# Optimization experiments

Hardware: AMD Instinct MI355X
Metric: run time of the kernel (lower is better)

## Reference

```python
import jax, jax.numpy as jnp
import numpy as np

N, D = 65536, 1024
EPS = 1e-12  # matches torch F.normalize default eps

def setup_inputs() -> dict:
    key = jax.random.key(0)
    k1, k2 = jax.random.split(key)
    premise = jax.random.normal(k1, (N, D), dtype=jnp.float32)
    hypothesis = jax.random.normal(k2, (N, D), dtype=jnp.float32)
    return {"premise": premise, "hypothesis": hypothesis}

def _l2_normalize(x):
    # torch.nn.functional.normalize(p=2, dim=-1): x / max(||x||, eps)
    norm = jnp.sqrt(jnp.sum(x * x, axis=-1, keepdims=True))
    return x / jnp.maximum(norm, EPS)

def reference(premise, hypothesis):
    # handle the [N,3,D] flattening branch of the original
    if premise.ndim == 3 and hypothesis.ndim == 3 and premise.shape[1] == 3 and hypothesis.shape[1] == 3:
        premise = premise.reshape(premise.shape[0], -1)
        hypothesis = hypothesis.reshape(hypothesis.shape[0], -1)
    p = _l2_normalize(premise)
    h = _l2_normalize(hypothesis)
    # diag(p @ h.T) == per-row dot product; avoid materializing NxN matrix
    return jnp.sum(p * h, axis=-1)
```

## Files before the change

### kernel.cpp

```cpp
#include <hip/hip_runtime.h>
#include <hip/hip_bf16.h>

#define D 1024
#define WAVES_PER_BLOCK 4

__global__ __launch_bounds__(256) void CosineSimilarity_76785425318088_kernel(
    const float* __restrict__ premise,
    const float* __restrict__ hypothesis,
    float* __restrict__ out,
    int n_rows) {
    const int wave = threadIdx.x >> 6;
    const int lane = threadIdx.x & 63;
    const int row = blockIdx.x * WAVES_PER_BLOCK + wave;
    if (row >= n_rows) return;

    const float4* __restrict__ prow = reinterpret_cast<const float4*>(premise    + (size_t)row * D);
    const float4* __restrict__ hrow = reinterpret_cast<const float4*>(hypothesis + (size_t)row * D);

    float dot = 0.f, pp = 0.f, hh = 0.f;
    #pragma unroll
    for (int j = 0; j < D / 4 / 64; ++j) {
        float4 a = prow[j * 64 + lane];
        float4 b = hrow[j * 64 + lane];
        dot = fmaf(a.x, b.x, dot); dot = fmaf(a.y, b.y, dot);
        dot = fmaf(a.z, b.z, dot); dot = fmaf(a.w, b.w, dot);
        pp  = fmaf(a.x, a.x, pp);  pp  = fmaf(a.y, a.y, pp);
        pp  = fmaf(a.z, a.z, pp);  pp  = fmaf(a.w, a.w, pp);
        hh  = fmaf(b.x, b.x, hh);  hh  = fmaf(b.y, b.y, hh);
        hh  = fmaf(b.z, b.z, hh);  hh  = fmaf(b.w, b.w, hh);
    }

    #pragma unroll
    for (int off = 32; off > 0; off >>= 1) {
        dot += __shfl_down(dot, off, 64);
        pp  += __shfl_down(pp,  off, 64);
        hh  += __shfl_down(hh,  off, 64);
    }

    if (lane == 0) {
        const float eps = 1e-12f;
        float denom = fmaxf(sqrtf(pp), eps) * fmaxf(sqrtf(hh), eps);
        out[row] = dot / denom;
    }
}

extern "C" void kernel_launch(void* const* d_in, const int* in_sizes, int n_in,
                              void* d_out, int out_size, void* d_ws, size_t ws_size,
                              hipStream_t stream) {
    const float* premise    = (const float*)d_in[0];
    const float* hypothesis = (const float*)d_in[1];
    float* out = (float*)d_out;
    const int n_rows = out_size;

    const int blocks = (n_rows + WAVES_PER_BLOCK - 1) / WAVES_PER_BLOCK;
    CosineSimilarity_76785425318088_kernel<<<blocks, 256, 0, stream>>>(
        premise, hypothesis, out, n_rows);
}
```

Baseline: 497.5 us.

## Use persistent grid-stride waves with register double-buffered nontemporal row loads

Replaces the one-row-per-wave launch with a fixed grid of 2048 blocks whose waves walk rows in a grid-stride loop. Each iteration prefetches the next row's eight float4 loads into registers before reducing the current row, and all loads are marked nontemporal. The aim is to overlap memory latency with the shuffle reduction and avoid cache pollution on a purely streaming 512MB read. The cost is double the register footprint and fewer waves in flight than the original launch.

```diff
diff --git a/kernel.cpp b/kernel.cpp
--- a/kernel.cpp
+++ b/kernel.cpp
@@ -1,46 +1,85 @@
 #include <hip/hip_runtime.h>
-#include <hip/hip_bf16.h>
 
 #define D 1024
-#define WAVES_PER_BLOCK 4
+#define TPB 256
+#define NBLOCKS 2048
 
-__global__ __launch_bounds__(256) void CosineSimilarity_76785425318088_kernel(
+typedef float f4 __attribute__((ext_vector_type(4)));
+
+__global__ __launch_bounds__(TPB, 4) void CosineSimilarity_76785425318088_kernel(
     const float* __restrict__ premise,
     const float* __restrict__ hypothesis,
     float* __restrict__ out,
     int n_rows) {
     const int wave = threadIdx.x >> 6;
     const int lane = threadIdx.x & 63;
-    const int row = blockIdx.x * WAVES_PER_BLOCK + wave;
+    const int waves_per_block = TPB >> 6;
+    const int nwaves = gridDim.x * waves_per_block;
+    int row = blockIdx.x * waves_per_block + wave;
     if (row >= n_rows) return;
 
-    const float4* __restrict__ prow = reinterpret_cast<const float4*>(premise    + (size_t)row * D);
-    const float4* __restrict__ hrow = reinterpret_cast<const float4*>(hypothesis + (size_t)row * D);
+    const f4* __restrict__ pbase = reinterpret_cast<const f4*>(premise);
+    const f4* __restrict__ hbase = reinterpret_cast<const f4*>(hypothesis);
+    const int QF = D / 4;
 
-    float dot = 0.f, pp = 0.f, hh = 0.f;
-    #pragma unroll
-    for (int j = 0; j < D / 4 / 64; ++j) {
-        float4 a = prow[j * 64 + lane];
-        float4 b = hrow[j * 64 + lane];
-        dot = fmaf(a.x, b.x, dot); dot = fmaf(a.y, b.y, dot);
-        dot = fmaf(a.z, b.z, dot); dot = fmaf(a.w, b.w, dot);
-        pp  = fmaf(a.x, a.x, pp);  pp  = fmaf(a.y, a.y, pp);
-        pp  = fmaf(a.z, a.z, pp);  pp  = fmaf(a.w, a.w, pp);
-        hh  = fmaf(b.x, b.x, hh);  hh  = fmaf(b.y, b.y, hh);
-        hh  = fmaf(b.z, b.z, hh);  hh  = fmaf(b.w, b.w, hh);
+    f4 pa0, pa1, pa2, pa3, pb0, pb1, pb2, pb3;
+    {
+        const f4* pr = pbase + (size_t)row * QF + lane;
+        const f4* hr = hbase + (size_t)row * QF + lane;
+        pa0 = __builtin_nontemporal_load(pr);
+        pb0 = __builtin_nontemporal_load(hr);
+        pa1 = __builtin_nontemporal_load(pr + 64);
+        pb1 = __builtin_nontemporal_load(hr + 64);
+        pa2 = __builtin_nontemporal_load(pr + 128);
+        pb2 = __builtin_nontemporal_load(hr + 128);
+        pa3 = __builtin_nontemporal_load(pr + 192);
+        pb3 = __builtin_nontemporal_load(hr + 192);
     }
 
-    #pragma unroll
-    for (int off = 32; off > 0; off >>= 1) {
-        dot += __shfl_down(dot, off, 64);
-        pp  += __shfl_down(pp,  off, 64);
-        hh  += __shfl_down(hh,  off, 64);
-    }
+    for (;;) {
+        const int nrow = row + nwaves;
+        const bool have_next = (nrow < n_rows);
 
-    if (lane == 0) {
-        const float eps = 1e-12f;
-        float denom = fmaxf(sqrtf(pp), eps) * fmaxf(sqrtf(hh), eps);
-        out[row] = dot / denom;
+        f4 na0, na1, na2, na3, nb0, nb1, nb2, nb3;
+        if (have_next) {
+            const f4* pr = pbase + (size_t)nrow * QF + lane;
+            const f4* hr = hbase + (size_t)nrow * QF + lane;
+            na0 = __builtin_nontemporal_load(pr);
+            nb0 = __builtin_nontemporal_load(hr);
+            na1 = __builtin_nontemporal_load(pr + 64);
+            nb1 = __builtin_nontemporal_load(hr + 64);
+            na2 = __builtin_nontemporal_load(pr + 128);
+            nb2 = __builtin_nontemporal_load(hr + 128);
+            na3 = __builtin_nontemporal_load(pr + 192);
+            nb3 = __builtin_nontemporal_load(hr + 192);
+        }
+
+        float dot = 0.f, pp = 0.f, hh = 0.f;
+#define ACC(A, B)                                                                  \
+        dot = fmaf(A.x, B.x, dot); pp = fmaf(A.x, A.x, pp); hh = fmaf(B.x, B.x, hh); \
+        dot = fmaf(A.y, B.y, dot); pp = fmaf(A.y, A.y, pp); hh = fmaf(B.y, B.y, hh); \
+        dot = fmaf(A.z, B.z, dot); pp = fmaf(A.z, A.z, pp); hh = fmaf(B.z, B.z, hh); \
+        dot = fmaf(A.w, B.w, dot); pp = fmaf(A.w, A.w, pp); hh = fmaf(B.w, B.w, hh);
+        ACC(pa0, pb0) ACC(pa1, pb1) ACC(pa2, pb2) ACC(pa3, pb3)
+#undef ACC
+
+#pragma unroll
+        for (int off = 32; off > 0; off >>= 1) {
+            dot += __shfl_down(dot, off, 64);
+            pp  += __shfl_down(pp,  off, 64);
+            hh  += __shfl_down(hh,  off, 64);
+        }
+
+        if (lane == 0) {
+            const float eps = 1e-12f;
+            float denom = fmaxf(sqrtf(pp), eps) * fmaxf(sqrtf(hh), eps);
+            out[row] = dot / denom;
+        }
+
+        if (!have_next) break;
+        row = nrow;
+        pa0 = na0; pa1 = na1; pa2 = na2; pa3 = na3;
+        pb0 = nb0; pb1 = nb1; pb2 = nb2; pb3 = nb3;
     }
 }
 
@@ -52,7 +91,11 @@
     float* out = (float*)d_out;
     const int n_rows = out_size;
 
-    const int blocks = (n_rows + WAVES_PER_BLOCK - 1) / WAVES_PER_BLOCK;
-    CosineSimilarity_76785425318088_kernel<<<blocks, 256, 0, stream>>>(
+    const int waves_per_block = TPB >> 6;
+    int blocks = NBLOCKS;
+    int max_useful = (n_rows + waves_per_block - 1) / waves_per_block;
+    if (blocks > max_useful) blocks = max_useful;
+
+    CosineSimilarity_76785425318088_kernel<<<blocks, TPB, 0, stream>>>(
         premise, hypothesis, out, n_rows);
 }
```

Result: faster. 467.4 us (-6.0%).

## Use persistent grid-stride waves with register double-buffered row prefetch

Applied to the files above, without the earlier changes.

Replaces the one-row-per-wave launch with a fixed grid of 2048 blocks. Each wave strides over rows and loads the next row's premise and hypothesis vectors into registers before reducing the current row. This aims to keep more memory requests in flight and overlap loads with the shuffle reduction. The cost is higher register use and fewer, longer-lived waves, which may reduce latency hiding if occupancy drops.

```diff
diff --git a/kernel.cpp b/kernel.cpp
--- a/kernel.cpp
+++ b/kernel.cpp
@@ -1,47 +1,82 @@
 #include <hip/hip_runtime.h>
-#include <hip/hip_bf16.h>
 
 #define D 1024
-#define WAVES_PER_BLOCK 4
+#define TPB 256
+#define NBLOCKS 2048
 
-__global__ __launch_bounds__(256) void CosineSimilarity_76785425318088_kernel(
-    const float* __restrict__ premise,
-    const float* __restrict__ hypothesis,
-    float* __restrict__ out,
-    int n_rows) {
-    const int wave = threadIdx.x >> 6;
-    const int lane = threadIdx.x & 63;
-    const int row = blockIdx.x * WAVES_PER_BLOCK + wave;
-    if (row >= n_rows) return;
+typedef float f4 __attribute__((ext_vector_type(4)));
 
-    const float4* __restrict__ prow = reinterpret_cast<const float4*>(premise    + (size_t)row * D);
-    const float4* __restrict__ hrow = reinterpret_cast<const float4*>(hypothesis + (size_t)row * D);
+__device__ __forceinline__ void row_finish(
+    f4 a0, f4 a1, f4 a2, f4 a3,
+    f4 b0, f4 b1, f4 b2, f4 b3,
+    int lane, float* __restrict__ out, int row) {
+    float dot = 0.f, pp = 0.f, hh = 0.f;
+#define ACC(A, B)                                                                    \
+    dot = fmaf(A.x, B.x, dot); pp = fmaf(A.x, A.x, pp); hh = fmaf(B.x, B.x, hh);     \
+    dot = fmaf(A.y, B.y, dot); pp = fmaf(A.y, A.y, pp); hh = fmaf(B.y, B.y, hh);     \
+    dot = fmaf(A.z, B.z, dot); pp = fmaf(A.z, A.z, pp); hh = fmaf(B.z, B.z, hh);     \
+    dot = fmaf(A.w, B.w, dot); pp = fmaf(A.w, A.w, pp); hh = fmaf(B.w, B.w, hh);
+    ACC(a0, b0) ACC(a1, b1) ACC(a2, b2) ACC(a3, b3)
+#undef ACC
 
-    float dot = 0.f, pp = 0.f, hh = 0.f;
-    #pragma unroll
-    for (int j = 0; j < D / 4 / 64; ++j) {
-        float4 a = prow[j * 64 + lane];
-        float4 b = hrow[j * 64 + lane];
-        dot = fmaf(a.x, b.x, dot); dot = fmaf(a.y, b.y, dot);
-        dot = fmaf(a.z, b.z, dot); dot = fmaf(a.w, b.w, dot);
-        pp  = fmaf(a.x, a.x, pp);  pp  = fmaf(a.y, a.y, pp);
-        pp  = fmaf(a.z, a.z, pp);  pp  = fmaf(a.w, a.w, pp);
-        hh  = fmaf(b.x, b.x, hh);  hh  = fmaf(b.y, b.y, hh);
-        hh  = fmaf(b.z, b.z, hh);  hh  = fmaf(b.w, b.w, hh);
-    }
-
-    #pragma unroll
+#pragma unroll
     for (int off = 32; off > 0; off >>= 1) {
         dot += __shfl_down(dot, off, 64);
         pp  += __shfl_down(pp,  off, 64);
         hh  += __shfl_down(hh,  off, 64);
     }
-
     if (lane == 0) {
         const float eps = 1e-12f;
         float denom = fmaxf(sqrtf(pp), eps) * fmaxf(sqrtf(hh), eps);
         out[row] = dot / denom;
     }
+}
+
+__global__ __launch_bounds__(TPB, 4) void CosineSimilarity_76785425318088_kernel(
+    const float* __restrict__ premise,
+    const float* __restrict__ hypothesis,
+    float* __restrict__ out,
+    int n_rows) {
+    const int lane = threadIdx.x & 63;
+    const int wave = threadIdx.x >> 6;
+    const int wpb  = TPB >> 6;
+    const int S    = gridDim.x * wpb;
+    const int row0 = blockIdx.x * wpb + wave;
+    if (row0 >= n_rows) return;
+    const int my_rows = (n_rows - 1 - row0) / S + 1;
+
+    const f4* __restrict__ pbase = reinterpret_cast<const f4*>(premise);
+    const f4* __restrict__ hbase = reinterpret_cast<const f4*>(hypothesis);
+    const int QF = D / 4;
+
+    f4 a0, a1, a2, a3, b0, b1, b2, b3;
+    {
+        const f4* pr = pbase + (size_t)row0 * QF + lane;
+        const f4* hr = hbase + (size_t)row0 * QF + lane;
+        a0 = pr[0];   b0 = hr[0];
+        a1 = pr[64];  b1 = hr[64];
+        a2 = pr[128]; b2 = hr[128];
+        a3 = pr[192]; b3 = hr[192];
+    }
+
+    int row = row0;
+    for (int i = 1; i < my_rows; ++i) {
+        const int nrow = row0 + i * S;
+        const f4* pr = pbase + (size_t)nrow * QF + lane;
+        const f4* hr = hbase + (size_t)nrow * QF + lane;
+        f4 na0 = pr[0],   nb0 = hr[0];
+        f4 na1 = pr[64],  nb1 = hr[64];
+        f4 na2 = pr[128], nb2 = hr[128];
+        f4 na3 = pr[192], nb3 = hr[192];
+
+        row_finish(a0, a1, a2, a3, b0, b1, b2, b3, lane, out, row);
+
+        row = nrow;
+        a0 = na0; a1 = na1; a2 = na2; a3 = na3;
+        b0 = nb0; b1 = nb1; b2 = nb2; b3 = nb3;
+    }
+
+    row_finish(a0, a1, a2, a3, b0, b1, b2, b3, lane, out, row);
 }
 
 extern "C" void kernel_launch(void* const* d_in, const int* in_sizes, int n_in,
@@ -52,7 +87,11 @@
     float* out = (float*)d_out;
     const int n_rows = out_size;
 
-    const int blocks = (n_rows + WAVES_PER_BLOCK - 1) / WAVES_PER_BLOCK;
-    CosineSimilarity_76785425318088_kernel<<<blocks, 256, 0, stream>>>(
+    const int wpb = TPB >> 6;
+    int blocks = NBLOCKS;
+    int max_useful = (n_rows + wpb - 1) / wpb;
+    if (blocks > max_useful) blocks = max_useful;
+
+    CosineSimilarity_76785425318088_kernel<<<blocks, TPB, 0, stream>>>(
         premise, hypothesis, out, n_rows);
 }
```

After: 498.2 us. Within noise of the previous version (+0.2%).
